# Kernel tuning notes

Hardware: AMD Instinct MI355X
Metric: run time of the kernel (lower is better)

The kernel has to match this reference:

```python
import jax, jax.numpy as jnp
import numpy as np

ALPHA = 0.5  # ent message step size
BETA = 0.5   # rel message step size
N_ENT, N_REL, D, E = 100000, 500, 128, 1000000
EPS = 1e-12  # tf.math.l2_normalize epsilon


def _mul_complex(x, y):
    # interleaved complex multiply: even idx = real, odd idx = imag (RotatE)
    xr, xi = x[:, ::2], x[:, 1::2]
    yr, yi = y[:, ::2], y[:, 1::2]
    rr = xr * yr - xi * yi
    ri = xi * yr + xr * yi
    return jnp.stack([rr, ri], axis=2).reshape(x.shape[0], -1)


def _l2_normalize_pairs(r):
    # tf.math.l2_normalize over each (real, imag) pair
    r2 = r.reshape(-1, 2)
    denom = jnp.sqrt(jnp.maximum(jnp.sum(r2 * r2, axis=1, keepdims=True), EPS))
    return (r2 / denom).reshape(r.shape)


def setup_inputs() -> dict:
    key = jax.random.key(0)
    k = jax.random.split(key, 7)
    return {
        "ent_emb": jax.random.normal(k[0], (N_ENT, D), dtype=jnp.float32),
        "rel_emb": jax.random.normal(k[1], (N_REL, D), dtype=jnp.float32),
        "ent_invsum": jax.random.uniform(k[2], (N_ENT, 1), dtype=jnp.float32),
        "rel_invsum": jax.random.uniform(k[3], (N_REL, 1), dtype=jnp.float32),
        "head": jax.random.randint(k[4], (E,), 0, N_ENT, dtype=jnp.int32),
        "rel_idx": jax.random.randint(k[5], (E,), 0, N_REL, dtype=jnp.int32),
        "tail": jax.random.randint(k[6], (E,), 0, N_ENT, dtype=jnp.int32),
    }


def reference(ent_emb, rel_emb, ent_invsum, rel_invsum, head, rel_idx, tail):
    # RotatE mode: normalize each complex component of relation embeddings
    rel_n = _l2_normalize_pairs(rel_emb)

    def loss_fn(e, r):
        h = e[head]            # [E, D] gather
        t = e[tail]            # [E, D] gather
        rg = r[rel_idx]        # [E, D] gather
        return -jnp.sum((_mul_complex(h, rg) - t) ** 2)

    # tf.gradients(loss, [ent_emb, rel_emb]) -> scatter-add messages
    ent_msg, rel_msg = jax.grad(loss_fn, argnums=(0, 1))(ent_emb, rel_n)

    out_ent = jax.nn.relu(ent_emb + ALPHA * ent_invsum * ent_msg)
    out_rel = jax.nn.relu(rel_n + BETA * rel_invsum * rel_msg)
    return out_ent, out_rel
```

## Files before the change

### kernel.cpp

```cpp
#include <hip/hip_runtime.h>

#define N_ENT   100000
#define N_REL   500
#define DIM     128
#define NPAIR   64
#define CAP_E   36
#define NREP    8
#define CAP_RR  344
#define BIN_SH  5
#define NBIN    (N_ENT >> BIN_SH)
#define CAP_B   152
#define BS_THR  1024
#define MAXE    4
#define NCOPY   8
#define ALPHA   0.5f
#define BETA    0.5f
#define EPS_N   1e-12f
#define PMASK   0x1FFFFu
#define PAYMASK 0x03FFFFFFu
#define INVALID 0xFFFFFFFFu

typedef float v2f __attribute__((ext_vector_type(2)));

__device__ __forceinline__ unsigned get_xcc() {
    unsigned x;
    asm("s_getreg_b32 %0, hwreg(HW_REG_XCC_ID)" : "=s"(x));
    return x & (NREP - 1u);
}

__device__ __forceinline__ unsigned pack_bf16(float2 v) {
    unsigned rx = __float_as_uint(v.x);
    unsigned ry = __float_as_uint(v.y);
    rx = (rx + 0x7FFFu + ((rx >> 16) & 1u)) >> 16;
    ry = (ry + 0x7FFFu + ((ry >> 16) & 1u)) & 0xFFFF0000u;
    return rx | ry;
}
__device__ __forceinline__ float2 unpack_bf16(unsigned u) {
    float2 v;
    v.x = __uint_as_float(u << 16);
    v.y = __uint_as_float(u & 0xFFFF0000u);
    return v;
}

__device__ __forceinline__ float2 unpack_fp8(unsigned short u) {
    v2f r = __builtin_amdgcn_cvt_pk_f32_fp8((int)u, false);
    return make_float2(r[0], r[1]);
}

__global__ void zero_kernel(float* p, int n) {
    int i = blockIdx.x * blockDim.x + threadIdx.x;
    if (i < n) p[i] = 0.0f;
}

__global__ void cvt_ent_kernel(const float* __restrict__ ent, unsigned* __restrict__ ent_f8, int ndw) {
    int i = blockIdx.x * blockDim.x + threadIdx.x;
    if (i >= ndw) return;
    float4 v = reinterpret_cast<const float4*>(ent)[i];
    int p = __builtin_amdgcn_cvt_pk_fp8_f32(v.x, v.y, 0, false);
    p = __builtin_amdgcn_cvt_pk_fp8_f32(v.z, v.w, p, true);
    ent_f8[i] = (unsigned)p;
}

__global__ void rel_norm_kernel(const float* __restrict__ rel, float* __restrict__ rel_n,
                                unsigned* __restrict__ rel_bf, int npairs) {
    int i = blockIdx.x * blockDim.x + threadIdx.x;
    if (i >= npairs) return;
    float2 v = reinterpret_cast<const float2*>(rel)[i];
    float d = sqrtf(fmaxf(v.x * v.x + v.y * v.y, EPS_N));
    float2 o; o.x = v.x / d; o.y = v.y / d;
    reinterpret_cast<float2*>(rel_n)[i] = o;
    rel_bf[i] = pack_bf16(o);
}


__global__ __launch_bounds__(BS_THR) void bin_scatter(
                            const int* __restrict__ head,
                            const int* __restrict__ relidx,
                            const int* __restrict__ tail,
                            unsigned* __restrict__ bin_cnt,
                            unsigned* __restrict__ bins,
                            unsigned* __restrict__ deg_r,
                            uint2*    __restrict__ list_r,
                            int n_edge) {
    __shared__ unsigned lcnt[NBIN];
    __shared__ unsigned lbase[NBIN];
    __shared__ unsigned rcnt[N_REL];
    __shared__ unsigned rbase[N_REL];
    int tid = threadIdx.x;

    for (int i = tid; i < NBIN; i += BS_THR) lcnt[i] = 0;
    for (int i = tid; i < N_REL; i += BS_THR) rcnt[i] = 0;
    __syncthreads();

    int e0 = blockIdx.x * (MAXE * BS_THR);

    unsigned eh[MAXE], er[MAXE], et[MAXE];
#pragma unroll
    for (int i = 0; i < MAXE; ++i) {
        int e = e0 + tid + i * BS_THR;
        if (e < n_edge) {
            eh[i] = (unsigned)head[e];
            er[i] = (unsigned)relidx[e];
            et[i] = (unsigned)tail[e];
        } else {
            eh[i] = INVALID; er[i] = 0; et[i] = 0;
        }
    }

#pragma unroll
    for (int i = 0; i < MAXE; ++i) {
        if (eh[i] != INVALID) {
            atomicAdd(&lcnt[et[i] >> BIN_SH], 1u);
            atomicAdd(&lcnt[eh[i] >> BIN_SH], 1u);
            atomicAdd(&rcnt[er[i]], 1u);
        }
    }
    __syncthreads();

    unsigned rep = get_xcc();
    for (int b = tid; b < NBIN; b += BS_THR) {
        unsigned c = lcnt[b];
        if (c) lbase[b] = __hip_atomic_fetch_add(&bin_cnt[rep * NBIN + b], c,
                                                 __ATOMIC_RELAXED, __HIP_MEMORY_SCOPE_WORKGROUP);
    }
    for (int b = tid; b < N_REL; b += BS_THR) {
        unsigned c = rcnt[b];
        if (c) rbase[b] = __hip_atomic_fetch_add(&deg_r[rep * N_REL + b], c,
                                                 __ATOMIC_RELAXED, __HIP_MEMORY_SCOPE_WORKGROUP);
    }
    __syncthreads();

#pragma unroll
    for (int i = 0; i < MAXE; ++i) {
        if (eh[i] == INVALID) continue;
        unsigned h = eh[i], r = er[i], t = et[i];

        unsigned bt = t >> BIN_SH;
        unsigned s1 = lbase[bt] + (atomicSub(&lcnt[bt], 1u) - 1u);
        if (s1 < CAP_B) bins[((size_t)rep * NBIN + bt) * CAP_B + s1] = ((t & 31u) << 27) | (r << 17) | h;

        unsigned bh = h >> BIN_SH;
        unsigned s2 = lbase[bh] + (atomicSub(&lcnt[bh], 1u) - 1u);
        if (s2 < CAP_B) bins[((size_t)rep * NBIN + bh) * CAP_B + s2] = ((h & 31u) << 27) | (1u << 26) | (r << 17) | t;

        unsigned s3 = rbase[r] + (atomicSub(&rcnt[r], 1u) - 1u);
        if (s3 < CAP_RR) list_r[((size_t)rep * N_REL + r) * CAP_RR + s3] = make_uint2(h, t);
    }
}

__global__ void fused_ent(const float* __restrict__ ent,
                          const unsigned short* __restrict__ ent_f8,
                          const unsigned* __restrict__ rel_bf,
                          const unsigned* __restrict__ bin_cnt,
                          const unsigned* __restrict__ bins,
                          const float* __restrict__ ent_inv,
                          float* __restrict__ out_ent) {
    __shared__ unsigned cnt[32][2];
    __shared__ unsigned slots[32][2][CAP_E];
    int bin = blockIdx.x;
    int tid = threadIdx.x;

    if (tid < 64) cnt[tid >> 1][tid & 1] = 0;
    __syncthreads();

    for (int rep = 0; rep < NREP; ++rep) {
        int bn = (int)min(bin_cnt[(size_t)rep * NBIN + bin], (unsigned)CAP_B);
        for (int k = tid; k < bn; k += blockDim.x) {
            unsigned entry = bins[((size_t)rep * NBIN + bin) * CAP_B + k];
            unsigned el   = entry >> 27;
            unsigned role = (entry >> 26) & 1u;
            unsigned pay  = entry & PAYMASK;
            unsigned p = atomicAdd(&cnt[el][role], 1u);
            if (p < CAP_E) slots[el][role][p] = pay;
        }
    }
    __syncthreads();

    int wid  = tid >> 6;
    int lane = tid & 63;
    const float2* ent2 = reinterpret_cast<const float2*>(ent);

    for (int s = 0; s < 8; ++s) {
        int el = wid * 8 + s;
        int e  = (bin << BIN_SH) + el;
        int dt = (int)min(cnt[el][0], (unsigned)CAP_E);
        int dh = (int)min(cnt[el][1], (unsigned)CAP_E);

        float2 acc = make_float2(0.f, 0.f);
        for (int j = 0; j < dt; ++j) {
            unsigned ep = slots[el][0][j];
            float2 hv = unpack_fp8(ent_f8[(size_t)(ep & PMASK) * NPAIR + lane]);
            float2 rv = unpack_bf16(rel_bf[(size_t)(ep >> 17) * NPAIR + lane]);
            acc.x += hv.x * rv.x - hv.y * rv.y;
            acc.y += hv.y * rv.x + hv.x * rv.y;
        }
        for (int j = 0; j < dh; ++j) {
            unsigned ep = slots[el][1][j];
            float2 tv = unpack_fp8(ent_f8[(size_t)(ep & PMASK) * NPAIR + lane]);
            float2 rv = unpack_bf16(rel_bf[(size_t)(ep >> 17) * NPAIR + lane]);
            acc.x += tv.x * rv.x + tv.y * rv.y;
            acc.y += tv.y * rv.x - tv.x * rv.y;
        }

        float2 ev = ent2[(size_t)e * NPAIR + lane];
        float degf = (float)(dt + dh);
        float a = ALPHA * ent_inv[e];
        float2 o;
        o.x = fmaxf(ev.x + a * 2.f * (acc.x - degf * ev.x), 0.f);
        o.y = fmaxf(ev.y + a * 2.f * (acc.y - degf * ev.y), 0.f);
        reinterpret_cast<float2*>(out_ent)[(size_t)e * NPAIR + lane] = o;
    }
}

__global__ void rel_pass8(const unsigned short* __restrict__ ent_f8,
                          const unsigned* __restrict__ deg_r,
                          const uint2* __restrict__ list_r,
                          float* __restrict__ rel_part) {
    __shared__ float sh[4][NPAIR][3];
    int r   = blockIdx.x >> 3;
    int rep = blockIdx.x & 7;
    int wid = threadIdx.x >> 6;
    int lane = threadIdx.x & 63;
    int nr = (int)min(deg_r[(size_t)rep * N_REL + r], (unsigned)CAP_RR);

    const uint2* seg = list_r + ((size_t)rep * N_REL + r) * CAP_RR;

    float2 T0 = make_float2(0.f, 0.f), T1 = make_float2(0.f, 0.f);
    float S0 = 0.f, S1 = 0.f;
    for (int k = wid * 2; k < nr; k += 8) {
        uint2 e0 = seg[k];
        float2 hv0 = unpack_fp8(ent_f8[(size_t)e0.x * NPAIR + lane]);
        float2 tv0 = unpack_fp8(ent_f8[(size_t)e0.y * NPAIR + lane]);
        if (k + 1 < nr) {
            uint2 e1 = seg[k + 1];
            float2 hv1 = unpack_fp8(ent_f8[(size_t)e1.x * NPAIR + lane]);
            float2 tv1 = unpack_fp8(ent_f8[(size_t)e1.y * NPAIR + lane]);
            S1   += hv1.x * hv1.x + hv1.y * hv1.y;
            T1.x += tv1.x * hv1.x + tv1.y * hv1.y;
            T1.y += tv1.y * hv1.x - tv1.x * hv1.y;
        }
        S0   += hv0.x * hv0.x + hv0.y * hv0.y;
        T0.x += tv0.x * hv0.x + tv0.y * hv0.y;
        T0.y += tv0.y * hv0.x - tv0.x * hv0.y;
    }
    sh[wid][lane][0] = T0.x + T1.x;
    sh[wid][lane][1] = T0.y + T1.y;
    sh[wid][lane][2] = S0 + S1;
    __syncthreads();
    if (wid == 0) {
        float tx = 0.f, ty = 0.f, s = 0.f;
#pragma unroll
        for (int w = 0; w < 4; ++w) {
            tx += sh[w][lane][0];
            ty += sh[w][lane][1];
            s  += sh[w][lane][2];
        }
        size_t o = (((size_t)r * NREP + rep) * NPAIR + lane) * 3;
        rel_part[o + 0] = tx;
        rel_part[o + 1] = ty;
        rel_part[o + 2] = s;
    }
}

__global__ void rel_fin(const float* __restrict__ rel_n,
                        const float* __restrict__ rel_part,
                        const float* __restrict__ rel_inv,
                        float* __restrict__ out_rel) {
    int r = blockIdx.x;
    int lane = threadIdx.x;
    float tx = 0.f, ty = 0.f, s = 0.f;
#pragma unroll
    for (int rep = 0; rep < NREP; ++rep) {
        size_t o = (((size_t)r * NREP + rep) * NPAIR + lane) * 3;
        tx += rel_part[o + 0];
        ty += rel_part[o + 1];
        s  += rel_part[o + 2];
    }
    float2 rn = reinterpret_cast<const float2*>(rel_n)[(size_t)r * NPAIR + lane];
    float b = BETA * rel_inv[r];
    float2 o2;
    o2.x = fmaxf(rn.x + b * (-2.f) * (rn.x * s - tx), 0.f);
    o2.y = fmaxf(rn.y + b * (-2.f) * (rn.y * s - ty), 0.f);
    reinterpret_cast<float2*>(out_rel)[(size_t)r * NPAIR + lane] = o2;
}


__global__ void rel_norm_only(const float* __restrict__ rel, float* __restrict__ rel_n, int npairs) {
    int i = blockIdx.x * blockDim.x + threadIdx.x;
    if (i >= npairs) return;
    float2 v = reinterpret_cast<const float2*>(rel)[i];
    float d = sqrtf(fmaxf(v.x * v.x + v.y * v.y, EPS_N));
    float2 o; o.x = v.x / d; o.y = v.y / d;
    reinterpret_cast<float2*>(rel_n)[i] = o;
}

__global__ void edge_kernel(const float* __restrict__ ent,
                            const float* __restrict__ rel_n,
                            const int* __restrict__ head,
                            const int* __restrict__ relidx,
                            const int* __restrict__ tail,
                            float* __restrict__ ent_msg,
                            float* __restrict__ rel_msg,
                            int n_edge) {
    int gid  = blockIdx.x * blockDim.x + threadIdx.x;
    int eid  = gid >> 6;
    int lane = threadIdx.x & 63;
    if (eid >= n_edge) return;

    int h = head[eid];
    int t = tail[eid];
    int r = relidx[eid];

    float2 hv = reinterpret_cast<const float2*>(ent)[(size_t)h * 64 + lane];
    float2 tv = reinterpret_cast<const float2*>(ent)[(size_t)t * 64 + lane];
    float2 rv = reinterpret_cast<const float2*>(rel_n)[(size_t)r * 64 + lane];

    float mr = hv.x * rv.x - hv.y * rv.y;
    float mi = hv.y * rv.x + hv.x * rv.y;
    float dr = mr - tv.x;
    float di = mi - tv.y;

    atomicAdd(&ent_msg[(size_t)t * DIM + 2 * lane],     2.0f * dr);
    atomicAdd(&ent_msg[(size_t)t * DIM + 2 * lane + 1], 2.0f * di);
    atomicAdd(&ent_msg[(size_t)h * DIM + 2 * lane],     -2.0f * (dr * rv.x + di * rv.y));
    atomicAdd(&ent_msg[(size_t)h * DIM + 2 * lane + 1], -2.0f * (di * rv.x - dr * rv.y));

    float* rm = rel_msg + (size_t)(blockIdx.x & (NCOPY - 1)) * (N_REL * DIM);
    atomicAdd(&rm[(size_t)r * DIM + 2 * lane],     -2.0f * (dr * hv.x + di * hv.y));
    atomicAdd(&rm[(size_t)r * DIM + 2 * lane + 1], -2.0f * (di * hv.x - dr * hv.y));
}

__global__ void fin_ent_kernel(const float* __restrict__ ent,
                               const float* __restrict__ invsum,
                               float* __restrict__ out, int nvec4) {
    int i = blockIdx.x * blockDim.x + threadIdx.x;
    if (i >= nvec4) return;
    int row = i >> 5;
    float a = ALPHA * invsum[row];
    float4 m = reinterpret_cast<const float4*>(out)[i];
    float4 e = reinterpret_cast<const float4*>(ent)[i];
    float4 o;
    o.x = fmaxf(e.x + a * m.x, 0.0f);
    o.y = fmaxf(e.y + a * m.y, 0.0f);
    o.z = fmaxf(e.z + a * m.z, 0.0f);
    o.w = fmaxf(e.w + a * m.w, 0.0f);
    reinterpret_cast<float4*>(out)[i] = o;
}

__global__ void fin_rel_kernel(const float* __restrict__ rel_n,
                               const float* __restrict__ invsum,
                               const float* __restrict__ rel_msg,
                               float* __restrict__ out, int n) {
    int i = blockIdx.x * blockDim.x + threadIdx.x;
    if (i >= n) return;
    int row = i >> 7;
    float s = 0.0f;
#pragma unroll
    for (int c = 0; c < NCOPY; ++c) s += rel_msg[(size_t)c * (N_REL * DIM) + i];
    float o = rel_n[i] + BETA * invsum[row] * s;
    out[i] = fmaxf(o, 0.0f);
}

extern "C" void kernel_launch(void* const* d_in, const int* in_sizes, int n_in,
                              void* d_out, int out_size, void* d_ws, size_t ws_size,
                              hipStream_t stream) {
    const float* ent     = (const float*)d_in[0];
    const float* rel     = (const float*)d_in[1];
    const float* ent_inv = (const float*)d_in[2];
    const float* rel_inv = (const float*)d_in[3];
    const int*   head    = (const int*)d_in[4];
    const int*   relidx  = (const int*)d_in[5];
    const int*   tail    = (const int*)d_in[6];

    const int n_edge = in_sizes[4];

    float* out     = (float*)d_out;
    float* out_ent = out;
    float* out_rel = out + (size_t)N_ENT * DIM;

    const int B = 256;

    const size_t W_RELN  = 0;
    const size_t W_RELB  = W_RELN + (size_t)N_REL * NPAIR * 2;
    const size_t W_ENTF8 = W_RELB + (size_t)N_REL * NPAIR;
    const size_t W_BCNT  = W_ENTF8 + (size_t)N_ENT * NPAIR / 2;
    const size_t W_DEGR  = W_BCNT + (size_t)NREP * NBIN;
    const size_t W_RPART = W_DEGR + (size_t)NREP * N_REL;
    const size_t W_BINS  = W_RPART + (size_t)N_REL * NREP * NPAIR * 3;
    const size_t W_LISTR = W_BINS + (size_t)NREP * NBIN * CAP_B;
    const size_t W_END   = W_LISTR + (size_t)NREP * N_REL * CAP_RR * 2;
    const size_t need_fast = W_END * 4;

    float* ws = (float*)d_ws;

    if (ws_size >= need_fast) {
        float*          rel_n    = ws + W_RELN;
        unsigned*       rel_bf   = (unsigned*)(ws + W_RELB);
        unsigned short* ent_f8   = (unsigned short*)(ws + W_ENTF8);
        unsigned*       bin_cnt  = (unsigned*)(ws + W_BCNT);
        unsigned*       deg_r    = (unsigned*)(ws + W_DEGR);
        float*          rel_part = ws + W_RPART;
        unsigned*       bins     = (unsigned*)(ws + W_BINS);
        uint2*          list_r   = (uint2*)(ws + W_LISTR);

        hipMemsetAsync((void*)bin_cnt, 0,
                       (size_t)(NREP * NBIN + NREP * N_REL) * 4, stream);

        {
            int ndw = N_ENT * DIM / 4;
            cvt_ent_kernel<<<(ndw + B - 1) / B, B, 0, stream>>>(ent, (unsigned*)ent_f8, ndw);
        }
        {
            int npairs = N_REL * NPAIR;
            rel_norm_kernel<<<(npairs + B - 1) / B, B, 0, stream>>>(rel, rel_n, rel_bf, npairs);
        }
        {
            int nblk = (n_edge + MAXE * BS_THR - 1) / (MAXE * BS_THR);
            bin_scatter<<<nblk, BS_THR, 0, stream>>>(
                head, relidx, tail, bin_cnt, bins, deg_r, list_r, n_edge);
        }

        fused_ent<<<NBIN, B, 0, stream>>>(ent, ent_f8, rel_bf, bin_cnt, bins,
                                          ent_inv, out_ent);
        rel_pass8<<<N_REL * NREP, B, 0, stream>>>(ent_f8, deg_r, list_r, rel_part);
        rel_fin<<<N_REL, 64, 0, stream>>>(rel_n, rel_part, rel_inv, out_rel);
    } else {
        float* rel_n   = ws;
        float* rel_msg = ws + N_REL * DIM;

        {
            int n = N_ENT * DIM;
            zero_kernel<<<(n + B - 1) / B, B, 0, stream>>>(out_ent, n);
            int m = NCOPY * N_REL * DIM;
            zero_kernel<<<(m + B - 1) / B, B, 0, stream>>>(rel_msg, m);
        }
        {
            int npairs = N_REL * NPAIR;
            rel_norm_only<<<(npairs + B - 1) / B, B, 0, stream>>>(rel, rel_n, npairs);
        }
        {
            long long threads = (long long)n_edge * 64;
            int blocks = (int)((threads + B - 1) / B);
            edge_kernel<<<blocks, B, 0, stream>>>(ent, rel_n, head, relidx, tail,
                                                  out_ent, rel_msg, n_edge);
        }
        {
            int nvec4 = N_ENT * (DIM / 4);
            fin_ent_kernel<<<(nvec4 + B - 1) / B, B, 0, stream>>>(ent, ent_inv, out_ent, nvec4);
            int n = N_REL * DIM;
            fin_rel_kernel<<<(n + B - 1) / B, B, 0, stream>>>(rel_n, rel_inv, rel_msg, out_rel, n);
        }
    }
}
```

Before: 207.2 us.

## Merge independent producer and consumer kernels into two block-partitioned launches

The entity fp8 conversion, relation normalization and edge bin-scatter now run as one launch, with the block index range split between the three jobs. The entity-update and relation-partial kernels are likewise merged into one launch partitioned by block index. This removes launch gaps and lets the independent work overlap instead of running back to back. In exchange, the conversion blocks now run at 1024 threads and reserve the scatter kernel's large shared-memory footprint, which may lower occupancy. The consumer blocks also carry the union of both kernels' shared memory.

```diff
diff --git a/kernel.cpp b/kernel.cpp
--- a/kernel.cpp
+++ b/kernel.cpp
@@ -52,41 +52,50 @@
     if (i < n) p[i] = 0.0f;
 }
 
-__global__ void cvt_ent_kernel(const float* __restrict__ ent, unsigned* __restrict__ ent_f8, int ndw) {
-    int i = blockIdx.x * blockDim.x + threadIdx.x;
-    if (i >= ndw) return;
-    float4 v = reinterpret_cast<const float4*>(ent)[i];
-    int p = __builtin_amdgcn_cvt_pk_fp8_f32(v.x, v.y, 0, false);
-    p = __builtin_amdgcn_cvt_pk_fp8_f32(v.z, v.w, p, true);
-    ent_f8[i] = (unsigned)p;
-}
-
-__global__ void rel_norm_kernel(const float* __restrict__ rel, float* __restrict__ rel_n,
-                                unsigned* __restrict__ rel_bf, int npairs) {
-    int i = blockIdx.x * blockDim.x + threadIdx.x;
-    if (i >= npairs) return;
-    float2 v = reinterpret_cast<const float2*>(rel)[i];
-    float d = sqrtf(fmaxf(v.x * v.x + v.y * v.y, EPS_N));
-    float2 o; o.x = v.x / d; o.y = v.y / d;
-    reinterpret_cast<float2*>(rel_n)[i] = o;
-    rel_bf[i] = pack_bf16(o);
-}
-
-
-__global__ __launch_bounds__(BS_THR) void bin_scatter(
+__global__ __launch_bounds__(BS_THR) void build_all(
                             const int* __restrict__ head,
                             const int* __restrict__ relidx,
                             const int* __restrict__ tail,
+                            const float* __restrict__ ent,
+                            const float* __restrict__ rel,
                             unsigned* __restrict__ bin_cnt,
                             unsigned* __restrict__ bins,
                             unsigned* __restrict__ deg_r,
                             uint2*    __restrict__ list_r,
-                            int n_edge) {
+                            unsigned* __restrict__ ent_f8,
+                            float*    __restrict__ rel_n,
+                            unsigned* __restrict__ rel_bf,
+                            int n_edge, int scat_blks, int cvt_blks) {
     __shared__ unsigned lcnt[NBIN];
     __shared__ unsigned lbase[NBIN];
     __shared__ unsigned rcnt[N_REL];
     __shared__ unsigned rbase[N_REL];
     int tid = threadIdx.x;
+
+    if ((int)blockIdx.x >= scat_blks) {
+        int cb = (int)blockIdx.x - scat_blks;
+        if (cb < cvt_blks) {
+            int i = cb * BS_THR + tid;
+            int ndw = N_ENT * DIM / 4;
+            if (i < ndw) {
+                float4 v = reinterpret_cast<const float4*>(ent)[i];
+                int p = __builtin_amdgcn_cvt_pk_fp8_f32(v.x, v.y, 0, false);
+                p = __builtin_amdgcn_cvt_pk_fp8_f32(v.z, v.w, p, true);
+                ent_f8[i] = (unsigned)p;
+            }
+        } else {
+            int i = (cb - cvt_blks) * BS_THR + tid;
+            int npairs = N_REL * NPAIR;
+            if (i < npairs) {
+                float2 v = reinterpret_cast<const float2*>(rel)[i];
+                float d = sqrtf(fmaxf(v.x * v.x + v.y * v.y, EPS_N));
+                float2 o; o.x = v.x / d; o.y = v.y / d;
+                reinterpret_cast<float2*>(rel_n)[i] = o;
+                rel_bf[i] = pack_bf16(o);
+            }
+        }
+        return;
+    }
 
     for (int i = tid; i < NBIN; i += BS_THR) lcnt[i] = 0;
     for (int i = tid; i < N_REL; i += BS_THR) rcnt[i] = 0;
@@ -148,17 +157,70 @@
     }
 }
 
-__global__ void fused_ent(const float* __restrict__ ent,
-                          const unsigned short* __restrict__ ent_f8,
-                          const unsigned* __restrict__ rel_bf,
-                          const unsigned* __restrict__ bin_cnt,
-                          const unsigned* __restrict__ bins,
-                          const float* __restrict__ ent_inv,
-                          float* __restrict__ out_ent) {
+__global__ void consume_all(const float* __restrict__ ent,
+                            const unsigned short* __restrict__ ent_f8,
+                            const unsigned* __restrict__ rel_bf,
+                            const unsigned* __restrict__ bin_cnt,
+                            const unsigned* __restrict__ bins,
+                            const float* __restrict__ ent_inv,
+                            const unsigned* __restrict__ deg_r,
+                            const uint2* __restrict__ list_r,
+                            float* __restrict__ rel_part,
+                            float* __restrict__ out_ent) {
     __shared__ unsigned cnt[32][2];
     __shared__ unsigned slots[32][2][CAP_E];
+    __shared__ float sh[4][NPAIR][3];
+    int tid = threadIdx.x;
+
+    if ((int)blockIdx.x >= NBIN) {
+        int idx = (int)blockIdx.x - NBIN;
+        int r   = idx >> 3;
+        int rep = idx & 7;
+        int wid = tid >> 6;
+        int lane = tid & 63;
+        int nr = (int)min(deg_r[(size_t)rep * N_REL + r], (unsigned)CAP_RR);
+
+        const uint2* seg = list_r + ((size_t)rep * N_REL + r) * CAP_RR;
+
+        float2 T0 = make_float2(0.f, 0.f), T1 = make_float2(0.f, 0.f);
+        float S0 = 0.f, S1 = 0.f;
+        for (int k = wid * 2; k < nr; k += 8) {
+            uint2 e0 = seg[k];
+            float2 hv0 = unpack_fp8(ent_f8[(size_t)e0.x * NPAIR + lane]);
+            float2 tv0 = unpack_fp8(ent_f8[(size_t)e0.y * NPAIR + lane]);
+            if (k + 1 < nr) {
+                uint2 e1 = seg[k + 1];
+                float2 hv1 = unpack_fp8(ent_f8[(size_t)e1.x * NPAIR + lane]);
+                float2 tv1 = unpack_fp8(ent_f8[(size_t)e1.y * NPAIR + lane]);
+                S1   += hv1.x * hv1.x + hv1.y * hv1.y;
+                T1.x += tv1.x * hv1.x + tv1.y * hv1.y;
+                T1.y += tv1.y * hv1.x - tv1.x * hv1.y;
+            }
+            S0   += hv0.x * hv0.x + hv0.y * hv0.y;
+            T0.x += tv0.x * hv0.x + tv0.y * hv0.y;
+            T0.y += tv0.y * hv0.x - tv0.x * hv0.y;
+        }
+        sh[wid][lane][0] = T0.x + T1.x;
+        sh[wid][lane][1] = T0.y + T1.y;
+        sh[wid][lane][2] = S0 + S1;
+        __syncthreads();
+        if (wid == 0) {
+            float tx = 0.f, ty = 0.f, s = 0.f;
+#pragma unroll
+            for (int w = 0; w < 4; ++w) {
+                tx += sh[w][lane][0];
+                ty += sh[w][lane][1];
+                s  += sh[w][lane][2];
+            }
+            size_t o = (((size_t)r * NREP + rep) * NPAIR + lane) * 3;
+            rel_part[o + 0] = tx;
+            rel_part[o + 1] = ty;
+            rel_part[o + 2] = s;
+        }
+        return;
+    }
+
     int bin = blockIdx.x;
-    int tid = threadIdx.x;
 
     if (tid < 64) cnt[tid >> 1][tid & 1] = 0;
     __syncthreads();
@@ -209,56 +271,6 @@
         o.x = fmaxf(ev.x + a * 2.f * (acc.x - degf * ev.x), 0.f);
         o.y = fmaxf(ev.y + a * 2.f * (acc.y - degf * ev.y), 0.f);
         reinterpret_cast<float2*>(out_ent)[(size_t)e * NPAIR + lane] = o;
-    }
-}
-
-__global__ void rel_pass8(const unsigned short* __restrict__ ent_f8,
-                          const unsigned* __restrict__ deg_r,
-                          const uint2* __restrict__ list_r,
-                          float* __restrict__ rel_part) {
-    __shared__ float sh[4][NPAIR][3];
-    int r   = blockIdx.x >> 3;
-    int rep = blockIdx.x & 7;
-    int wid = threadIdx.x >> 6;
-    int lane = threadIdx.x & 63;
-    int nr = (int)min(deg_r[(size_t)rep * N_REL + r], (unsigned)CAP_RR);
-
-    const uint2* seg = list_r + ((size_t)rep * N_REL + r) * CAP_RR;
-
-    float2 T0 = make_float2(0.f, 0.f), T1 = make_float2(0.f, 0.f);
-    float S0 = 0.f, S1 = 0.f;
-    for (int k = wid * 2; k < nr; k += 8) {
-        uint2 e0 = seg[k];
-        float2 hv0 = unpack_fp8(ent_f8[(size_t)e0.x * NPAIR + lane]);
-        float2 tv0 = unpack_fp8(ent_f8[(size_t)e0.y * NPAIR + lane]);
-        if (k + 1 < nr) {
-            uint2 e1 = seg[k + 1];
-            float2 hv1 = unpack_fp8(ent_f8[(size_t)e1.x * NPAIR + lane]);
-            float2 tv1 = unpack_fp8(ent_f8[(size_t)e1.y * NPAIR + lane]);
-            S1   += hv1.x * hv1.x + hv1.y * hv1.y;
-            T1.x += tv1.x * hv1.x + tv1.y * hv1.y;
-            T1.y += tv1.y * hv1.x - tv1.x * hv1.y;
-        }
-        S0   += hv0.x * hv0.x + hv0.y * hv0.y;
-        T0.x += tv0.x * hv0.x + tv0.y * hv0.y;
-        T0.y += tv0.y * hv0.x - tv0.x * hv0.y;
-    }
-    sh[wid][lane][0] = T0.x + T1.x;
-    sh[wid][lane][1] = T0.y + T1.y;
-    sh[wid][lane][2] = S0 + S1;
-    __syncthreads();
-    if (wid == 0) {
-        float tx = 0.f, ty = 0.f, s = 0.f;
-#pragma unroll
-        for (int w = 0; w < 4; ++w) {
-            tx += sh[w][lane][0];
-            ty += sh[w][lane][1];
-            s  += sh[w][lane][2];
-        }
-        size_t o = (((size_t)r * NREP + rep) * NPAIR + lane) * 3;
-        rel_part[o + 0] = tx;
-        rel_part[o + 1] = ty;
-        rel_part[o + 2] = s;
     }
 }
 
@@ -407,22 +419,20 @@
                        (size_t)(NREP * NBIN + NREP * N_REL) * 4, stream);
 
         {
-            int ndw = N_ENT * DIM / 4;
-            cvt_ent_kernel<<<(ndw + B - 1) / B, B, 0, stream>>>(ent, (unsigned*)ent_f8, ndw);
-        }
-        {
-            int npairs = N_REL * NPAIR;
-            rel_norm_kernel<<<(npairs + B - 1) / B, B, 0, stream>>>(rel, rel_n, rel_bf, npairs);
-        }
-        {
-            int nblk = (n_edge + MAXE * BS_THR - 1) / (MAXE * BS_THR);
-            bin_scatter<<<nblk, BS_THR, 0, stream>>>(
-                head, relidx, tail, bin_cnt, bins, deg_r, list_r, n_edge);
-        }
-
-        fused_ent<<<NBIN, B, 0, stream>>>(ent, ent_f8, rel_bf, bin_cnt, bins,
-                                          ent_inv, out_ent);
-        rel_pass8<<<N_REL * NREP, B, 0, stream>>>(ent_f8, deg_r, list_r, rel_part);
+            int scat_blks = (n_edge + MAXE * BS_THR - 1) / (MAXE * BS_THR);
+            int cvt_blks  = (N_ENT * DIM / 4 + BS_THR - 1) / BS_THR;
+            int rn_blks   = (N_REL * NPAIR + BS_THR - 1) / BS_THR;
+            build_all<<<scat_blks + cvt_blks + rn_blks, BS_THR, 0, stream>>>(
+                head, relidx, tail, ent, rel,
+                bin_cnt, bins, deg_r, list_r,
+                (unsigned*)ent_f8, rel_n, rel_bf,
+                n_edge, scat_blks, cvt_blks);
+        }
+
+        consume_all<<<NBIN + N_REL * NREP, B, 0, stream>>>(
+            ent, ent_f8, rel_bf, bin_cnt, bins, ent_inv,
+            deg_r, list_r, rel_part, out_ent);
+
         rel_fin<<<N_REL, 64, 0, stream>>>(rel_n, rel_part, rel_inv, out_rel);
     } else {
         float* rel_n   = ws;
```

New measurement: 191.9 us, median of 2. -7.4%, faster.
